# Kernel optimization log

Measured on AMD Instinct MI355X. Metric: run time of the kernel, lower is better.

## Reference

```python
import jax, jax.numpy as jnp
import numpy as np

B, L, D_MODEL = 2, 2048, 1024
D_STATE, D_CONV, EXPAND, DT_RANK = 16, 4, 2, 64
D_INNER = EXPAND * D_MODEL


def setup_inputs() -> dict:
    key = jax.random.key(0)
    ks = jax.random.split(key, 12)
    s = 0.02
    A_log = jnp.log(jnp.broadcast_to(jnp.arange(1, D_STATE + 1, dtype=jnp.float32), (D_INNER, D_STATE)))
    return {
        "x": jax.random.normal(ks[0], (B, L, D_MODEL), jnp.float32),
        "W_in": jax.random.normal(ks[1], (2 * D_INNER, D_MODEL), jnp.float32) * s,
        "conv_w": jax.random.normal(ks[2], (D_INNER, 1, D_CONV), jnp.float32) * 0.2,
        "conv_b": jax.random.normal(ks[3], (D_INNER,), jnp.float32) * s,
        "W_xp": jax.random.normal(ks[4], (DT_RANK + 2 * D_STATE, D_INNER), jnp.float32) * s,
        "W_dt": jax.random.normal(ks[5], (D_INNER, DT_RANK), jnp.float32) * 0.1,
        "b_dt": jax.random.uniform(ks[6], (D_INNER,), jnp.float32, -4.6, -2.3),  # ~softplus^-1 of small dt
        "A_log": A_log,
        "D": jnp.ones((D_INNER,), jnp.float32),
        "W_out_ssm": jax.random.normal(ks[7], (D_MODEL, D_INNER), jnp.float32) * s,
        "W_out": jax.random.normal(ks[8], (D_MODEL, D_MODEL), jnp.float32) * s,
        "b_out": jnp.zeros((D_MODEL,), jnp.float32),
    }


def _mamba_block(x, W_in, conv_w, conv_b, W_xp, W_dt, b_dt, A_log, D, W_out_ssm, W_out, b_out):
    d_inner = conv_b.shape[0]
    d_state = A_log.shape[1]
    dt_rank = W_dt.shape[1]
    d_conv = conv_w.shape[-1]

    # in_proj -> x branch and gate z
    xz = x @ W_in.T                         # [B, L, 2*d_inner]
    xin, z = jnp.split(xz, 2, axis=-1)

    # causal depthwise conv over time
    xc = jnp.transpose(xin, (0, 2, 1))      # [B, d_inner, L]
    xc = jax.lax.conv_general_dilated(
        xc, conv_w, window_strides=(1,), padding=[(d_conv - 1, 0)],
        feature_group_count=d_inner)
    xc = jax.nn.silu(xc + conv_b[None, :, None])
    xs = jnp.transpose(xc, (0, 2, 1))       # [B, L, d_inner]

    # input-dependent dt, B, C
    x_dbl = xs @ W_xp.T                     # [B, L, dt_rank + 2*d_state]
    dt, Bm, Cm = jnp.split(x_dbl, [dt_rank, dt_rank + d_state], axis=-1)
    dt = jax.nn.softplus(dt @ W_dt.T + b_dt)  # [B, L, d_inner]

    A = -jnp.exp(A_log)                     # [d_inner, d_state]

    def step(h, inp):
        dt_t, B_t, C_t, x_t = inp           # [B,di] [B,ds] [B,ds] [B,di]
        dA = jnp.exp(dt_t[:, :, None] * A)                      # [B, di, ds]
        h = h * dA + (dt_t * x_t)[:, :, None] * B_t[:, None, :]  # [B, di, ds]
        y = jnp.einsum('bds,bs->bd', h, C_t)
        return h, y

    h0 = jnp.zeros((x.shape[0], d_inner, d_state), x.dtype)
    tm = lambda a: jnp.swapaxes(a, 0, 1)    # time-major
    _, ys = jax.lax.scan(step, h0, (tm(dt), tm(Bm), tm(Cm), tm(xs)))
    y = jnp.swapaxes(ys, 0, 1)              # [B, L, d_inner]

    y = y + xs * D
    y = y * jax.nn.silu(z)
    y = y @ W_out_ssm.T                     # mamba-internal out_proj -> d_model
    return y @ W_out.T + b_out              # wrapper out_proj


def reference(x, W_in, conv_w, conv_b, W_xp, W_dt, b_dt, A_log, D, W_out_ssm, W_out, b_out):
    return _mamba_block(x, W_in, conv_w, conv_b, W_xp, W_dt, b_dt, A_log, D, W_out_ssm, W_out, b_out)
```

## Files before the change

### kernel.cpp

```cpp
#include <hip/hip_runtime.h>
#include <hip/hip_bf16.h>
#include <cmath>
#include <cstdint>

typedef __bf16 bf16_t;
typedef bf16_t bf16x8 __attribute__((ext_vector_type(8)));
typedef bf16_t bf16x4 __attribute__((ext_vector_type(4)));
typedef float f32x4 __attribute__((ext_vector_type(4)));

#define BB 2
#define LL 2048
#define DMODEL 1024
#define DINNER 2048
#define DSTATE 16
#define NC 64
#define CHUNK 32
#define KSEG 256

#define EXP2F(x) __builtin_amdgcn_exp2f(x)

#define CVT_N0 1048576
#define CVT_N1 2097152
#define CVT_N2 2129920
#define CVT_N3 2392064
#define CVT_NB0 9344
#define CVT_NB1 10368
#define CVT_NBT 10880
__global__ __launch_bounds__(256) void k_cvt_all(
    const float* __restrict__ x, const float* __restrict__ Win,
    const float* __restrict__ Wdt, const float* __restrict__ Wo,
    const float* __restrict__ Wxp, const float* __restrict__ Wos,
    bf16_t* __restrict__ x_b, bf16_t* __restrict__ Win_b,
    bf16_t* __restrict__ Wdt_b, bf16_t* __restrict__ Wo_b,
    bf16_t* __restrict__ Wxp_b, bf16_t* __restrict__ WosT_b) {
    const int tid = threadIdx.x;
    if (blockIdx.x < CVT_NB0) {
        int i = blockIdx.x * 256 + tid;
        const float* src; bf16_t* dst; int j;
        if (i < CVT_N0)      { src = x;   dst = x_b;   j = i; }
        else if (i < CVT_N1) { src = Win; dst = Win_b; j = i - CVT_N0; }
        else if (i < CVT_N2) { src = Wdt; dst = Wdt_b; j = i - CVT_N1; }
        else                 { src = Wo;  dst = Wo_b;  j = i - CVT_N2; }
        float4 v = reinterpret_cast<const float4*>(src)[j];
        bf16x4 o;
        o[0] = (bf16_t)v.x; o[1] = (bf16_t)v.y; o[2] = (bf16_t)v.z; o[3] = (bf16_t)v.w;
        reinterpret_cast<bf16x4*>(dst)[j] = o;
    } else if (blockIdx.x < CVT_NB1) {
        int i = (blockIdx.x - CVT_NB0) * 256 + tid;
        int r = i >> 11, c = i & (DINNER - 1);
        float v = (r < 96) ? Wxp[r * DINNER + c] : 0.f;
        Wxp_b[i] = (bf16_t)v;
    } else {
        __shared__ float tile[64][65];
        const int bid = blockIdx.x - CVT_NB1;
        const int m0 = (bid & 15) * 64;
        const int d0 = (bid >> 4) * 64;
        const int dl = tid & 63;
        #pragma unroll 4
        for (int i = 0; i < 16; ++i) {
            const int mr = (tid >> 6) + i * 4;
            tile[dl][mr] = Wos[(size_t)(m0 + mr) * DINNER + d0 + dl];
        }
        __syncthreads();
        const int dr = tid >> 2;
        const int q  = tid & 3;
        bf16_t* op = WosT_b + (size_t)(d0 + dr) * DMODEL + m0 + q * 16;
        bf16x8 v0, v1;
        #pragma unroll
        for (int j = 0; j < 8; ++j) v0[j] = (bf16_t)tile[dr][q * 16 + j];
        #pragma unroll
        for (int j = 0; j < 8; ++j) v1[j] = (bf16_t)tile[dr][q * 16 + 8 + j];
        reinterpret_cast<bf16x8*>(op)[0] = v0;
        reinterpret_cast<bf16x8*>(op)[1] = v1;
    }
}

__device__ __forceinline__ void gload16(const void* g, void* l) {
    __builtin_amdgcn_global_load_lds(
        (const __attribute__((address_space(1))) void*)g,
        (__attribute__((address_space(3))) void*)l,
        16, 0, 0);
}

__global__ __launch_bounds__(512) void k_gemm256(
    const bf16_t* __restrict__ x_b, const bf16_t* __restrict__ Win_b,
    bf16_t* __restrict__ xin_b, bf16_t* __restrict__ zsT) {
    __shared__ bf16_t lds[65536];
    const int tid = threadIdx.x;
    const int wid = tid >> 6, lane = tid & 63;

    const int bid = (blockIdx.x & 7) * 32 + (blockIdx.x >> 3);
    const bf16_t* A; const bf16_t* Bt; int m0, n0, sub;
    if (bid < 128) {
        sub = 0; A = x_b; Bt = Win_b;
        m0 = (bid >> 3) * 256; n0 = (bid & 7) * 256;
    } else {
        sub = 1; A = Win_b + (size_t)DINNER * DMODEL; Bt = x_b;
        const int t2 = bid - 128;
        m0 = (t2 >> 4) * 256; n0 = (t2 & 15) * 256;
    }
    const int wr = wid >> 2, wc = wid & 3;
    f32x4 acc[8][4] = {};

    const int srow = tid >> 3;
    const int k8p = (tid & 7) ^ (srow & 7);
    const bf16_t* apA = A + (size_t)(m0 + srow) * 1024 + k8p * 8;
    const bf16_t* apB = Bt + (size_t)(n0 + srow) * 1024 + k8p * 8;

    auto stageA = [&](int slot, int kt) {
        char* b0 = (char*)lds + slot * 32768 + wid * 1024;
        const bf16_t* src = apA + kt * 64;
        gload16(src, b0);
        gload16(src + (size_t)64 * 1024, b0 + 8192);
        gload16(src + (size_t)128 * 1024, b0 + 16384);
        gload16(src + (size_t)192 * 1024, b0 + 24576);
    };
    auto stageB = [&](int slot, int kt) {
        char* b0 = (char*)lds + 65536 + slot * 32768 + wid * 1024;
        const bf16_t* src = apB + kt * 64;
        gload16(src, b0);
        gload16(src + (size_t)64 * 1024, b0 + 8192);
        gload16(src + (size_t)128 * 1024, b0 + 16384);
        gload16(src + (size_t)192 * 1024, b0 + 24576);
    };

    const int lm = lane & 15, lq = lane >> 4;

    const bf16_t* pA0[8]; const bf16_t* pA1[8];
    const bf16_t* pB0[4]; const bf16_t* pB1[4];
    #pragma unroll
    for (int i = 0; i < 8; ++i) {
        const int rr = lm + i * 16;
        const int e0 = wr * 8192 + rr * 64 + (lq ^ (rr & 7)) * 8;
        pA0[i] = lds + e0;
        pA1[i] = lds + (e0 ^ 32);
    }
    #pragma unroll
    for (int j = 0; j < 4; ++j) {
        const int rr = (wc & 1) * 64 + lm + j * 16;
        const int e0 = 32768 + (wc >> 1) * 8192 + rr * 64 + (lq ^ (rr & 7)) * 8;
        pB0[j] = lds + e0;
        pB1[j] = lds + (e0 ^ 32);
    }

    auto body = [&](int t, int s) {
        asm volatile("s_waitcnt vmcnt(0)" ::: "memory");
        __builtin_amdgcn_sched_barrier(0);
        __builtin_amdgcn_s_barrier();
        __builtin_amdgcn_sched_barrier(0);
        if (t + 1 < 16) {
            stageA(s ^ 1, t + 1);
            stageB(s ^ 1, t + 1);
        }
        {
            bf16x8 fa[8], fb[4];
            #pragma unroll
            for (int i = 0; i < 8; ++i) fa[i] = *(const bf16x8*)(pA0[i] + s * 16384);
            #pragma unroll
            for (int j = 0; j < 4; ++j) fb[j] = *(const bf16x8*)(pB0[j] + s * 16384);
            __builtin_amdgcn_s_setprio(1);
            #pragma unroll
            for (int i = 0; i < 8; ++i)
                #pragma unroll
                for (int j = 0; j < 4; ++j)
                    acc[i][j] = __builtin_amdgcn_mfma_f32_16x16x32_bf16(fa[i], fb[j], acc[i][j], 0, 0, 0);
            __builtin_amdgcn_s_setprio(0);
        }
        {
            bf16x8 fa[8], fb[4];
            #pragma unroll
            for (int i = 0; i < 8; ++i) fa[i] = *(const bf16x8*)(pA1[i] + s * 16384);
            #pragma unroll
            for (int j = 0; j < 4; ++j) fb[j] = *(const bf16x8*)(pB1[j] + s * 16384);
            __builtin_amdgcn_s_setprio(1);
            #pragma unroll
            for (int i = 0; i < 8; ++i)
                #pragma unroll
                for (int j = 0; j < 4; ++j)
                    acc[i][j] = __builtin_amdgcn_mfma_f32_16x16x32_bf16(fa[i], fb[j], acc[i][j], 0, 0, 0);
            __builtin_amdgcn_s_setprio(0);
        }
    };

    stageA(0, 0);
    stageB(0, 0);
    for (int tt = 0; tt < 8; ++tt) {
        body(2 * tt, 0);
        body(2 * tt + 1, 1);
    }

    const int row0 = m0 + wr * 128 + lq * 4;
    const int col0 = n0 + wc * 64 + lm;
    #pragma unroll
    for (int i = 0; i < 8; ++i) {
        #pragma unroll
        for (int j = 0; j < 4; ++j) {
            #pragma unroll
            for (int r = 0; r < 4; ++r) {
                const int row = row0 + i * 16 + r;
                const int c = col0 + j * 16;
                float v = acc[i][j][r];
                if (sub == 0) xin_b[(size_t)row * DINNER + c] = (bf16_t)v;
                else          zsT[(size_t)row * (BB * LL) + c] = (bf16_t)(v / (1.f + __expf(-v)));
            }
        }
    }
}

enum { EPI_BF16 = 0, EPI_BIAS = 1, EPI_SOFTPLUS_RB = 3, EPI_PARTK = 4 };

template <int EPI>
__global__ __launch_bounds__(512) void k_gemm_cd128(
    const bf16_t* __restrict__ A, const bf16_t* __restrict__ Bt,
    int N, int Ktiles, int lda, int ldb,
    float* __restrict__ C, bf16_t* __restrict__ Cb,
    const float* __restrict__ bias) {
    __shared__ bf16_t lds[32768];
    const int tid = threadIdx.x;
    const int wid = tid >> 6, lane = tid & 63;
    const int bx = (blockIdx.x & 7) * ((int)gridDim.x >> 3) + (blockIdx.x >> 3);
    const int ntile = N >> 7;
    const int m0 = (bx / ntile) << 7;
    const int n0 = (bx % ntile) << 7;
    const int wr = wid >> 2, wc = wid & 3;
    f32x4 acc[4][2] = {};

    const int srow = tid >> 3;
    const int k8p = (tid & 7) ^ (srow & 7);
    const bf16_t* apA = A + (size_t)(m0 + srow) * lda + k8p * 8;
    const bf16_t* apB = Bt + (size_t)(n0 + srow) * ldb + k8p * 8;

    auto stageA = [&](int slot, int kt) {
        char* b0 = (char*)lds + slot * 16384 + wid * 1024;
        const bf16_t* src = apA + kt * 64;
        gload16(src, b0);
        gload16(src + (size_t)64 * lda, b0 + 8192);
    };
    auto stageB = [&](int slot, int kt) {
        char* b0 = (char*)lds + 32768 + slot * 16384 + wid * 1024;
        const bf16_t* src = apB + kt * 64;
        gload16(src, b0);
        gload16(src + (size_t)64 * ldb, b0 + 8192);
    };

    const int lm = lane & 15, lq = lane >> 4;

    const bf16_t* pA0[4]; const bf16_t* pA1[4];
    const bf16_t* pB0[2]; const bf16_t* pB1[2];
    #pragma unroll
    for (int i = 0; i < 4; ++i) {
        const int rr = lm + i * 16;
        const int e0 = wr * 4096 + rr * 64 + (lq ^ (rr & 7)) * 8;
        pA0[i] = lds + e0;
        pA1[i] = lds + (e0 ^ 32);
    }
    #pragma unroll
    for (int j = 0; j < 2; ++j) {
        const int rr = wc * 32 + lm + j * 16;
        const int e0 = 16384 + rr * 64 + (lq ^ (rr & 7)) * 8;
        pB0[j] = lds + e0;
        pB1[j] = lds + (e0 ^ 32);
    }

    auto body = [&](int t, int s) {
        asm volatile("s_waitcnt vmcnt(0)" ::: "memory");
        __builtin_amdgcn_sched_barrier(0);
        __builtin_amdgcn_s_barrier();
        __builtin_amdgcn_sched_barrier(0);
        if (t + 1 < Ktiles) {
            stageA(s ^ 1, t + 1);
            stageB(s ^ 1, t + 1);
        }
        {
            bf16x8 fa[4], fb[2];
            #pragma unroll
            for (int i = 0; i < 4; ++i) fa[i] = *(const bf16x8*)(pA0[i] + s * 8192);
            #pragma unroll
            for (int j = 0; j < 2; ++j) fb[j] = *(const bf16x8*)(pB0[j] + s * 8192);
            __builtin_amdgcn_s_setprio(1);
            #pragma unroll
            for (int i = 0; i < 4; ++i)
                #pragma unroll
                for (int j = 0; j < 2; ++j)
                    acc[i][j] = __builtin_amdgcn_mfma_f32_16x16x32_bf16(fa[i], fb[j], acc[i][j], 0, 0, 0);
            __builtin_amdgcn_s_setprio(0);
        }
        {
            bf16x8 fa[4], fb[2];
            #pragma unroll
            for (int i = 0; i < 4; ++i) fa[i] = *(const bf16x8*)(pA1[i] + s * 8192);
            #pragma unroll
            for (int j = 0; j < 2; ++j) fb[j] = *(const bf16x8*)(pB1[j] + s * 8192);
            __builtin_amdgcn_s_setprio(1);
            #pragma unroll
            for (int i = 0; i < 4; ++i)
                #pragma unroll
                for (int j = 0; j < 2; ++j)
                    acc[i][j] = __builtin_amdgcn_mfma_f32_16x16x32_bf16(fa[i], fb[j], acc[i][j], 0, 0, 0);
            __builtin_amdgcn_s_setprio(0);
        }
    };

    stageA(0, 0);
    stageB(0, 0);
    for (int tt = 0; tt < (Ktiles >> 1); ++tt) {
        body(2 * tt, 0);
        body(2 * tt + 1, 1);
    }

    const int row0 = m0 + wr * 64 + lq * 4;
    const int col0 = n0 + wc * 32 + lm;
    #pragma unroll
    for (int i = 0; i < 4; ++i) {
        #pragma unroll
        for (int j = 0; j < 2; ++j) {
            #pragma unroll
            for (int r = 0; r < 4; ++r) {
                const int row = row0 + i * 16 + r;
                const int c = col0 + j * 16;
                float v = acc[i][j][r];
                if (EPI == EPI_BF16) Cb[(size_t)row * N + c] = (bf16_t)v;
                else                 C[(size_t)row * N + c] = v + bias[c];
            }
        }
    }
}

template <int EPI>
__global__ __launch_bounds__(512) void k_gemm_bt(
    const bf16_t* __restrict__ A, const bf16_t* __restrict__ Bt,
    int M, int N, int Kloop, int lda, int ldb,
    float* __restrict__ C, bf16_t* __restrict__ Cb,
    const float* __restrict__ bias,
    bf16_t* __restrict__ o_part) {
    __shared__ bf16_t sA[2][128 * 32];
    __shared__ bf16_t sB[2][128 * 32];
    const int tid = threadIdx.x;
    const int wid = tid >> 6, lane = tid & 63;
    const int bx = (blockIdx.x & 7) * ((int)gridDim.x >> 3) + (blockIdx.x >> 3);
    int m0, n0, k0 = 0, seg = 0;
    if (EPI == EPI_PARTK) {
        m0 = (bx & 31) << 7;
        n0 = 0;
        seg = bx >> 5;
        k0 = seg * KSEG;
    } else {
        const int ntile = N >> 7;
        m0 = (bx / ntile) << 7;
        n0 = (bx % ntile) << 7;
    }
    const int wr = wid >> 2, wc = wid & 3;
    f32x4 acc[4][2] = {};

    const bf16_t* ap = A + (size_t)(m0 + (tid >> 2)) * lda + (tid & 3) * 8 + k0;
    const bf16_t* bp = Bt + (size_t)(n0 + (tid >> 2)) * ldb + (tid & 3) * 8 + k0;
    const int lm = lane & 15, lk = (lane >> 4) * 8;

    auto stage = [&](int buf, int kt) {
        char* dA = (char*)sA[buf] + wid * 1024;
        char* dB = (char*)sB[buf] + wid * 1024;
        gload16(ap + kt, dA);
        gload16(bp + kt, dB);
    };

    stage(0, 0);
    __syncthreads();
    int cur = 0;
    for (int kt = 0; kt < Kloop; kt += 32) {
        if (kt + 32 < Kloop) stage(cur ^ 1, kt + 32);
        const bf16_t* rA = sA[cur] + (wr * 64 + lm) * 32 + lk;
        const bf16_t* rB = sB[cur] + (wc * 32 + lm) * 32 + lk;
        bf16x8 fa[4], fb[2];
        #pragma unroll
        for (int i = 0; i < 4; ++i) fa[i] = *(const bf16x8*)(rA + i * 16 * 32);
        #pragma unroll
        for (int j = 0; j < 2; ++j) fb[j] = *(const bf16x8*)(rB + j * 16 * 32);
        __builtin_amdgcn_s_setprio(1);
        #pragma unroll
        for (int i = 0; i < 4; ++i)
            #pragma unroll
            for (int j = 0; j < 2; ++j)
                acc[i][j] = __builtin_amdgcn_mfma_f32_16x16x32_bf16(fa[i], fb[j], acc[i][j], 0, 0, 0);
        __builtin_amdgcn_s_setprio(0);
        __syncthreads();
        cur ^= 1;
    }

    const int row0 = m0 + wr * 64 + (lane >> 4) * 4;
    const int col0 = n0 + wc * 32 + lm;
    bf16_t* Cpb = (EPI == EPI_PARTK)
        ? o_part + (size_t)seg * ((size_t)4096 * 128)
        : nullptr;
    #pragma unroll
    for (int i = 0; i < 4; ++i) {
        #pragma unroll
        for (int j = 0; j < 2; ++j) {
            #pragma unroll
            for (int r = 0; r < 4; ++r) {
                int row = row0 + i * 16 + r;
                int c = col0 + j * 16;
                float v = acc[i][j][r];
                if (EPI == EPI_SOFTPLUS_RB) {
                    float xv = v + bias[row];
                    float sp = fmaxf(xv, 0.f) + log1pf(__expf(-fabsf(xv)));
                    Cb[(size_t)row * N + c] = (bf16_t)sp;
                } else {
                    Cpb[(size_t)row * 128 + c] = (bf16_t)v;
                }
            }
        }
    }
}

__global__ __launch_bounds__(256) void k_split_reduce(
    const bf16_t* __restrict__ part, bf16_t* __restrict__ dtr,
    float* __restrict__ Bmf, float* __restrict__ Cmf) {
    int idx = blockIdx.x * 256 + threadIdx.x;
    int row = idx >> 7, c = idx & 127;
    float s = 0.f;
    #pragma unroll
    for (int g = 0; g < 8; ++g) s += (float)part[(size_t)g * (4096 * 128) + idx];
    if (c < 64) dtr[(size_t)row * 64 + c] = (bf16_t)s;
    else if (c < 80) Bmf[(size_t)row * 16 + (c - 64)] = s;
    else if (c < 96) Cmf[(size_t)row * 16 + (c - 80)] = s;
}

__global__ __launch_bounds__(256) void k_conv(
    const bf16_t* __restrict__ xin, const float* __restrict__ cw,
    const float* __restrict__ cb, bf16_t* __restrict__ xs_b,
    bf16_t* __restrict__ xsT) {
    __shared__ float tile[64][65];
    const int tid = threadIdx.x;
    const int d0  = (blockIdx.x & 31) * 64;
    const int bl0 = (blockIdx.x >> 5) * 64;
    const int dl = tid & 63;
    const int d  = d0 + dl;
    const float w0 = cw[d * 4], w1 = cw[d * 4 + 1], w2 = cw[d * 4 + 2], w3 = cw[d * 4 + 3];
    const float bias = cb[d];
    const int l0 = bl0 & (LL - 1);
    #pragma unroll 4
    for (int i = 0; i < 16; ++i) {
        const int blr = (tid >> 6) + i * 4;
        const int bl = bl0 + blr;
        const int l  = l0 + blr;
        const bf16_t* rp = xin + (size_t)bl * DINNER + d;
        float acc = fmaf(w3, (float)rp[0], bias);
        if (l >= 1) acc = fmaf(w2, (float)rp[-(int)DINNER], acc);
        if (l >= 2) acc = fmaf(w1, (float)rp[-2 * (int)DINNER], acc);
        if (l >= 3) acc = fmaf(w0, (float)rp[-3 * (int)DINNER], acc);
        float sv = acc / (1.f + __expf(-acc));
        xs_b[(size_t)bl * DINNER + d] = (bf16_t)sv;
        tile[dl][blr] = sv;
    }
    __syncthreads();
    const int dr = tid >> 2;
    const int q  = tid & 3;
    bf16_t* op = xsT + (size_t)(d0 + dr) * (BB * LL) + bl0 + q * 16;
    bf16x8 v0, v1;
    #pragma unroll
    for (int j = 0; j < 8; ++j) v0[j] = (bf16_t)tile[dr][q * 16 + j];
    #pragma unroll
    for (int j = 0; j < 8; ++j) v1[j] = (bf16_t)tile[dr][q * 16 + 8 + j];
    reinterpret_cast<bf16x8*>(op)[0] = v0;
    reinterpret_cast<bf16x8*>(op)[1] = v1;
}


__global__ __launch_bounds__(256) void k_scan_p1(
    const bf16_t* __restrict__ dtT, const bf16_t* __restrict__ xsT,
    const float* __restrict__ Bm, const float* __restrict__ A_log,
    bf16_t* __restrict__ alpha, bf16_t* __restrict__ beta) {
    __shared__ float sB[CHUNK * 16];
    const int db = blockIdx.x & 7;
    const int ck = (blockIdx.x >> 3) & (NC - 1);
    const int b  = blockIdx.x >> 9;
    const int tid = threadIdx.x;
    const int d  = db * 256 + tid;
    const int t0 = ck * CHUNK;

    const float* Bsrc = Bm + ((size_t)b * LL + t0) * 16;
    sB[tid] = Bsrc[tid];
    sB[tid + 256] = Bsrc[tid + 256];

    f32x4 a2[4];
    #pragma unroll
    for (int q = 0; q < 4; ++q) {
        f32x4 av = reinterpret_cast<const f32x4*>(A_log + d * 16)[q];
        #pragma unroll
        for (int j = 0; j < 4; ++j) a2[q][j] = -__expf(av[j]) * 1.44269504f;
    }
    const bf16x8* dtp = reinterpret_cast<const bf16x8*>(dtT + (size_t)d * (BB * LL) + b * LL + t0);
    const bf16x8* xsp = reinterpret_cast<const bf16x8*>(xsT + (size_t)d * (BB * LL) + b * LL + t0);

    bf16x8 dtl[4], xsl[4];
    #pragma unroll
    for (int q = 0; q < 4; ++q) dtl[q] = dtp[q];
    #pragma unroll
    for (int q = 0; q < 4; ++q) xsl[q] = xsp[q];

    __syncthreads();

    float be[16];
    #pragma unroll
    for (int s = 0; s < 16; ++s) be[s] = 0.f;
    float dtsum = 0.f;

    #pragma unroll
    for (int t = 0; t < CHUNK; ++t) {
        float dtv = (float)dtl[t >> 3][t & 7];
        float xv  = (float)xsl[t >> 3][t & 7];
        float dtx = dtv * xv;
        dtsum += dtv;
        #pragma unroll
        for (int q = 0; q < 4; ++q) {
            f32x4 Bq = *reinterpret_cast<const f32x4*>(sB + t * 16 + q * 4);
            #pragma unroll
            for (int j = 0; j < 4; ++j) {
                const int s = q * 4 + j;
                float dA = EXP2F(dtv * a2[q][j]);
                be[s] = fmaf(be[s], dA, dtx * Bq[j]);
            }
        }
    }
    bf16_t* ap = alpha + ((size_t)(b * NC + ck)) * (DINNER * 16) + (size_t)d * 16;
    bf16_t* bp = beta  + ((size_t)(b * NC + ck)) * (DINNER * 16) + (size_t)d * 16;
    bf16x8 av0, av1, bv0, bv1;
    #pragma unroll
    for (int j = 0; j < 8; ++j) {
        av0[j] = (bf16_t)EXP2F(a2[j >> 2][j & 3] * dtsum);
        av1[j] = (bf16_t)EXP2F(a2[(j + 8) >> 2][j & 3] * dtsum);
        bv0[j] = (bf16_t)be[j];
        bv1[j] = (bf16_t)be[8 + j];
    }
    reinterpret_cast<bf16x8*>(ap)[0] = av0;
    reinterpret_cast<bf16x8*>(ap)[1] = av1;
    reinterpret_cast<bf16x8*>(bp)[0] = bv0;
    reinterpret_cast<bf16x8*>(bp)[1] = bv1;
}

__global__ __launch_bounds__(256) void k_scan_p2(
    const bf16_t* __restrict__ alpha, const bf16_t* __restrict__ beta,
    bf16_t* __restrict__ H) {
    const int gid = blockIdx.x * 256 + threadIdx.x;
    const int b = gid >> 15, r = gid & 32767;
    float h = 0.f;
    #pragma unroll 8
    for (int ck = 0; ck < NC; ++ck) {
        const size_t i = ((size_t)(b * NC + ck)) * 32768 + r;
        H[i] = (bf16_t)h;
        h = fmaf((float)alpha[i], h, (float)beta[i]);
    }
}

__global__ __launch_bounds__(256) void k_scan_p3(
    const bf16_t* __restrict__ dtT, const bf16_t* __restrict__ xsT,
    const float* __restrict__ Bm, const float* __restrict__ Cm,
    const bf16_t* __restrict__ zsT, const float* __restrict__ A_log,
    const float* __restrict__ Dp, const bf16_t* __restrict__ H,
    bf16_t* __restrict__ y) {
    __shared__ float sB[CHUNK * 16];
    __shared__ float sC[CHUNK * 16];
    const int db = blockIdx.x & 7;
    const int ck = (blockIdx.x >> 3) & (NC - 1);
    const int b  = blockIdx.x >> 9;
    const int tid = threadIdx.x;
    const int d  = db * 256 + tid;
    const int t0 = ck * CHUNK;

    const float* Bsrc = Bm + ((size_t)b * LL + t0) * 16;
    const float* Csrc = Cm + ((size_t)b * LL + t0) * 16;
    sB[tid] = Bsrc[tid];
    sB[tid + 256] = Bsrc[tid + 256];
    sC[tid] = Csrc[tid];
    sC[tid + 256] = Csrc[tid + 256];

    f32x4 a2[4];
    #pragma unroll
    for (int q = 0; q < 4; ++q) {
        f32x4 av = reinterpret_cast<const f32x4*>(A_log + d * 16)[q];
        #pragma unroll
        for (int j = 0; j < 4; ++j) a2[q][j] = -__expf(av[j]) * 1.44269504f;
    }
    const float Dd = Dp[d];
    const bf16x8* dtp = reinterpret_cast<const bf16x8*>(dtT + (size_t)d * (BB * LL) + b * LL + t0);
    const bf16x8* xsp = reinterpret_cast<const bf16x8*>(xsT + (size_t)d * (BB * LL) + b * LL + t0);
    const bf16x8* zp  = reinterpret_cast<const bf16x8*>(zsT + (size_t)d * (BB * LL) + b * LL + t0);
    bf16_t* yp = y + ((size_t)b * LL + t0) * DINNER + d;

    bf16x8 dtl[4], xsl[4], zsl[4];
    #pragma unroll
    for (int q = 0; q < 4; ++q) dtl[q] = dtp[q];
    #pragma unroll
    for (int q = 0; q < 4; ++q) xsl[q] = xsp[q];
    #pragma unroll
    for (int q = 0; q < 4; ++q) zsl[q] = zp[q];

    float h[16];
    {
        const bf16x8* hp = reinterpret_cast<const bf16x8*>(H + ((size_t)(b * NC + ck)) * 32768 + (size_t)d * 16);
        bf16x8 h0 = hp[0], h1 = hp[1];
        #pragma unroll
        for (int j = 0; j < 8; ++j) { h[j] = (float)h0[j]; h[8 + j] = (float)h1[j]; }
    }

    __syncthreads();

    #pragma unroll
    for (int t = 0; t < CHUNK; ++t) {
        float dtv = (float)dtl[t >> 3][t & 7];
        float xv  = (float)xsl[t >> 3][t & 7];
        float zv  = (float)zsl[t >> 3][t & 7];
        float dtx = dtv * xv;
        float yacc = 0.f;
        #pragma unroll
        for (int q = 0; q < 4; ++q) {
            f32x4 Bq = *reinterpret_cast<const f32x4*>(sB + t * 16 + q * 4);
            f32x4 Cq = *reinterpret_cast<const f32x4*>(sC + t * 16 + q * 4);
            #pragma unroll
            for (int j = 0; j < 4; ++j) {
                const int s = q * 4 + j;
                float dA = EXP2F(dtv * a2[q][j]);
                h[s] = fmaf(h[s], dA, dtx * Bq[j]);
                yacc = fmaf(h[s], Cq[j], yacc);
            }
        }
        float yv = (yacc + xv * Dd) * zv;
        yp[(size_t)t * DINNER] = (bf16_t)yv;
    }
}

extern "C" void kernel_launch(void* const* d_in, const int* in_sizes, int n_in,
                              void* d_out, int out_size, void* d_ws, size_t ws_size,
                              hipStream_t stream) {
    const float* x      = (const float*)d_in[0];
    const float* W_in   = (const float*)d_in[1];
    const float* conv_w = (const float*)d_in[2];
    const float* conv_b = (const float*)d_in[3];
    const float* W_xp   = (const float*)d_in[4];
    const float* W_dt   = (const float*)d_in[5];
    const float* b_dt   = (const float*)d_in[6];
    const float* A_log  = (const float*)d_in[7];
    const float* Dvec   = (const float*)d_in[8];
    const float* W_os   = (const float*)d_in[9];
    const float* W_o    = (const float*)d_in[10];
    const float* b_o    = (const float*)d_in[11];
    float* out = (float*)d_out;

    char* base = (char*)d_ws;
    size_t off = 0;
    auto alloc = [&](size_t bytes) -> char* {
        char* p = base + off;
        off += (bytes + 255) & ~(size_t)255;
        return p;
    };
    const int MR = BB * LL;
    bf16_t* x_b   = (bf16_t*)alloc((size_t)MR * DMODEL * 2);
    bf16_t* Win_b = (bf16_t*)alloc((size_t)4096 * 1024 * 2);
    bf16_t* xin_b = (bf16_t*)alloc((size_t)MR * DINNER * 2);
    bf16_t* xs_b  = (bf16_t*)alloc((size_t)MR * DINNER * 2);
    bf16_t* zsT   = (bf16_t*)alloc((size_t)DINNER * MR * 2);
    bf16_t* xsT   = (bf16_t*)alloc((size_t)DINNER * MR * 2);
    bf16_t* dtT_b = (bf16_t*)alloc((size_t)DINNER * MR * 2);
    float*  Hbuf  = (float*)alloc((size_t)BB * NC * DINNER * 16 * 4);
    bf16_t* y_b   = (bf16_t*)alloc((size_t)MR * DINNER * 2);
    bf16_t* dtr_b = (bf16_t*)alloc((size_t)MR * 64 * 2);
    float*  Bmf   = (float*)alloc((size_t)MR * 16 * 4);
    float*  Cmf   = (float*)alloc((size_t)MR * 16 * 4);
    bf16_t* Wxp_b = (bf16_t*)alloc((size_t)128 * DINNER * 2);
    bf16_t* Wdt_b = (bf16_t*)alloc((size_t)DINNER * 64 * 2);
    bf16_t* WosT_b= (bf16_t*)alloc((size_t)DINNER * DMODEL * 2);
    bf16_t* Wo_b  = (bf16_t*)alloc((size_t)DMODEL * DMODEL * 2);
    bf16_t* Wc_b  = (bf16_t*)alloc((size_t)DMODEL * DINNER * 2);

    bf16_t* alphab = (bf16_t*)xin_b;
    bf16_t* betab  = (bf16_t*)x_b;
    bf16_t* partk  = (bf16_t*)Hbuf;
    bf16_t* Hb     = (bf16_t*)Hbuf;

    k_cvt_all<<<CVT_NBT, 256, 0, stream>>>(
        x, W_in, W_dt, W_o, W_xp, W_os,
        x_b, Win_b, Wdt_b, Wo_b, Wxp_b, WosT_b);

    k_gemm_cd128<EPI_BF16><<<(DMODEL / 128) * (DINNER / 128), 512, 0, stream>>>(
        Wo_b, WosT_b, DINNER, 16, DMODEL, DMODEL, nullptr, Wc_b, nullptr);
    k_gemm256<<<256, 512, 0, stream>>>(x_b, Win_b, xin_b, zsT);
    k_conv<<<(MR / 64) * (DINNER / 64), 256, 0, stream>>>(xin_b, conv_w, conv_b, xs_b, xsT);
    k_gemm_bt<EPI_PARTK><<<8 * 32, 512, 0, stream>>>(
        xs_b, Wxp_b, MR, 128, KSEG, DINNER, DINNER,
        nullptr, nullptr, nullptr, partk);
    k_split_reduce<<<(MR * 128) / 256, 256, 0, stream>>>(partk, dtr_b, Bmf, Cmf);
    k_gemm_bt<EPI_SOFTPLUS_RB><<<(DINNER / 128) * (MR / 128), 512, 0, stream>>>(
        Wdt_b, dtr_b, DINNER, MR, 64, 64, 64,
        nullptr, dtT_b, b_dt, nullptr);
    k_scan_p1<<<BB * NC * (DINNER / 256), 256, 0, stream>>>(dtT_b, xsT, Bmf, A_log, alphab, betab);
    k_scan_p2<<<(BB * DINNER * DSTATE) / 256, 256, 0, stream>>>(alphab, betab, Hb);
    k_scan_p3<<<BB * NC * (DINNER / 256), 256, 0, stream>>>(dtT_b, xsT, Bmf, Cmf, zsT, A_log, Dvec, Hb, y_b);
    k_gemm_cd128<EPI_BIAS><<<(MR / 128) * (DMODEL / 128), 512, 0, stream>>>(
        y_b, Wc_b, DMODEL, 32, DINNER, DINNER, out, nullptr, b_o);
}
```

Before: 208.6 us.

## Fold weight-combine GEMM into in_proj GEMM launch as extra blocks

Merges the W_out·W_out_ssm precombination GEMM into the in_proj k_gemm256 launch: 128 additional blocks compute the 1024x2048 Wc product with a 128x128 tile path, and the grid grows from 256 to 384. This removes a separate kernel launch and lets both independent GEMMs share the device concurrently, filling CUs that the 256-block in_proj grid leaves idle. The cost is a heterogeneous kernel whose register and LDS footprint is set by the larger path, plus a changed block-to-tile mapping.

```diff
diff --git a/kernel.cpp b/kernel.cpp
--- a/kernel.cpp
+++ b/kernel.cpp
@@ -84,12 +84,121 @@
 
 __global__ __launch_bounds__(512) void k_gemm256(
     const bf16_t* __restrict__ x_b, const bf16_t* __restrict__ Win_b,
-    bf16_t* __restrict__ xin_b, bf16_t* __restrict__ zsT) {
+    const bf16_t* __restrict__ Wo_b, const bf16_t* __restrict__ WosT_b,
+    bf16_t* __restrict__ xin_b, bf16_t* __restrict__ zsT,
+    bf16_t* __restrict__ Wc_b) {
     __shared__ bf16_t lds[65536];
     const int tid = threadIdx.x;
     const int wid = tid >> 6, lane = tid & 63;
-
-    const int bid = (blockIdx.x & 7) * 32 + (blockIdx.x >> 3);
+    const int lm = lane & 15, lq = lane >> 4;
+
+    const int bid = (blockIdx.x & 7) * 48 + (blockIdx.x >> 3);
+
+    if (bid >= 256) {
+        const int t3 = bid - 256;
+        const int m0 = (t3 >> 4) << 7;
+        const int n0 = (t3 & 15) << 7;
+        const int wr = wid >> 2, wc = wid & 3;
+        f32x4 acc[4][2] = {};
+
+        const int srow = tid >> 3;
+        const int k8p = (tid & 7) ^ (srow & 7);
+        const bf16_t* apA = Wo_b + (size_t)(m0 + srow) * 1024 + k8p * 8;
+        const bf16_t* apB = WosT_b + (size_t)(n0 + srow) * 1024 + k8p * 8;
+
+        auto stageA = [&](int slot, int kt) {
+            char* b0 = (char*)lds + slot * 16384 + wid * 1024;
+            const bf16_t* src = apA + kt * 64;
+            gload16(src, b0);
+            gload16(src + (size_t)64 * 1024, b0 + 8192);
+        };
+        auto stageB = [&](int slot, int kt) {
+            char* b0 = (char*)lds + 32768 + slot * 16384 + wid * 1024;
+            const bf16_t* src = apB + kt * 64;
+            gload16(src, b0);
+            gload16(src + (size_t)64 * 1024, b0 + 8192);
+        };
+
+        const bf16_t* pA0[4]; const bf16_t* pA1[4];
+        const bf16_t* pB0[2]; const bf16_t* pB1[2];
+        #pragma unroll
+        for (int i = 0; i < 4; ++i) {
+            const int rr = lm + i * 16;
+            const int e0 = wr * 4096 + rr * 64 + (lq ^ (rr & 7)) * 8;
+            pA0[i] = lds + e0;
+            pA1[i] = lds + (e0 ^ 32);
+        }
+        #pragma unroll
+        for (int j = 0; j < 2; ++j) {
+            const int rr = wc * 32 + lm + j * 16;
+            const int e0 = 16384 + rr * 64 + (lq ^ (rr & 7)) * 8;
+            pB0[j] = lds + e0;
+            pB1[j] = lds + (e0 ^ 32);
+        }
+
+        auto body = [&](int t, int s) {
+            asm volatile("s_waitcnt vmcnt(0)" ::: "memory");
+            __builtin_amdgcn_sched_barrier(0);
+            __builtin_amdgcn_s_barrier();
+            __builtin_amdgcn_sched_barrier(0);
+            if (t + 1 < 16) {
+                stageA(s ^ 1, t + 1);
+                stageB(s ^ 1, t + 1);
+            }
+            {
+                bf16x8 fa[4], fb[2];
+                #pragma unroll
+                for (int i = 0; i < 4; ++i) fa[i] = *(const bf16x8*)(pA0[i] + s * 8192);
+                #pragma unroll
+                for (int j = 0; j < 2; ++j) fb[j] = *(const bf16x8*)(pB0[j] + s * 8192);
+                __builtin_amdgcn_s_setprio(1);
+                #pragma unroll
+                for (int i = 0; i < 4; ++i)
+                    #pragma unroll
+                    for (int j = 0; j < 2; ++j)
+                        acc[i][j] = __builtin_amdgcn_mfma_f32_16x16x32_bf16(fa[i], fb[j], acc[i][j], 0, 0, 0);
+                __builtin_amdgcn_s_setprio(0);
+            }
+            {
+                bf16x8 fa[4], fb[2];
+                #pragma unroll
+                for (int i = 0; i < 4; ++i) fa[i] = *(const bf16x8*)(pA1[i] + s * 8192);
+                #pragma unroll
+                for (int j = 0; j < 2; ++j) fb[j] = *(const bf16x8*)(pB1[j] + s * 8192);
+                __builtin_amdgcn_s_setprio(1);
+                #pragma unroll
+                for (int i = 0; i < 4; ++i)
+                    #pragma unroll
+                    for (int j = 0; j < 2; ++j)
+                        acc[i][j] = __builtin_amdgcn_mfma_f32_16x16x32_bf16(fa[i], fb[j], acc[i][j], 0, 0, 0);
+                __builtin_amdgcn_s_setprio(0);
+            }
+        };
+
+        stageA(0, 0);
+        stageB(0, 0);
+        for (int tt = 0; tt < 8; ++tt) {
+            body(2 * tt, 0);
+            body(2 * tt + 1, 1);
+        }
+
+        const int row0 = m0 + wr * 64 + lq * 4;
+        const int col0 = n0 + wc * 32 + lm;
+        #pragma unroll
+        for (int i = 0; i < 4; ++i) {
+            #pragma unroll
+            for (int j = 0; j < 2; ++j) {
+                #pragma unroll
+                for (int r = 0; r < 4; ++r) {
+                    const int row = row0 + i * 16 + r;
+                    const int c = col0 + j * 16;
+                    Wc_b[(size_t)row * DINNER + c] = (bf16_t)acc[i][j][r];
+                }
+            }
+        }
+        return;
+    }
+
     const bf16_t* A; const bf16_t* Bt; int m0, n0, sub;
     if (bid < 128) {
         sub = 0; A = x_b; Bt = Win_b;
@@ -123,8 +232,6 @@
         gload16(src + (size_t)128 * 1024, b0 + 16384);
         gload16(src + (size_t)192 * 1024, b0 + 24576);
     };
-
-    const int lm = lane & 15, lq = lane >> 4;
 
     const bf16_t* pA0[8]; const bf16_t* pA1[8];
     const bf16_t* pB0[4]; const bf16_t* pB1[4];
@@ -681,9 +788,8 @@
         x, W_in, W_dt, W_o, W_xp, W_os,
         x_b, Win_b, Wdt_b, Wo_b, Wxp_b, WosT_b);
 
-    k_gemm_cd128<EPI_BF16><<<(DMODEL / 128) * (DINNER / 128), 512, 0, stream>>>(
-        Wo_b, WosT_b, DINNER, 16, DMODEL, DMODEL, nullptr, Wc_b, nullptr);
-    k_gemm256<<<256, 512, 0, stream>>>(x_b, Win_b, xin_b, zsT);
+    k_gemm256<<<384, 512, 0, stream>>>(
+        x_b, Win_b, Wo_b, WosT_b, xin_b, zsT, Wc_b);
     k_conv<<<(MR / 64) * (DINNER / 64), 256, 0, stream>>>(xin_b, conv_w, conv_b, xs_b, xsT);
     k_gemm_bt<EPI_PARTK><<<8 * 32, 512, 0, stream>>>(
         xs_b, Wxp_b, MR, 128, KSEG, DINNER, DINNER,
```

New measurement: 225.2 us. 1.08x slower.
